# Performance work log

Hardware: AMD Instinct MI355X
Metric: run time of the kernel (lower is better)

## Reference

```python
import jax, jax.numpy as jnp
import numpy as np


def conv2d_nchw(x, w, b, padding):
    # x: [B,Cin,H,W], w: [Cout,Cin,kh,kw]
    y = jax.lax.conv_general_dilated(
        x, w, window_strides=(1, 1), padding=padding,
        dimension_numbers=("NCHW", "OIHW", "NCHW"))
    return y + b[None, :, None, None]


def setup_inputs() -> dict:
    key = jax.random.key(0)
    ks = jax.random.split(key, 8)
    B, C, H, W = 8, 512, 50, 76
    A = 9  # 3 scales x 3 ratios
    base_feat = jax.random.normal(ks[0], (B, C, H, W), dtype=jnp.float32)
    im_info = jnp.tile(jnp.array([800.0, 1216.0, 1.0], jnp.float32), (B, 1))
    gt_boxes = jax.random.uniform(ks[1], (B, 20, 5), dtype=jnp.float32) * 100.0
    num_boxes = jax.random.randint(ks[2], (B,), 1, 20, dtype=jnp.int32)
    # learned parameters (Kaiming-ish small init)
    conv_w = jax.random.normal(ks[3], (512, C, 3, 3), dtype=jnp.float32) * 0.01
    conv_b = jnp.zeros((512,), jnp.float32)
    cls_w = jax.random.normal(ks[4], (2 * A, 512, 1, 1), dtype=jnp.float32) * 0.01
    cls_b = jnp.zeros((2 * A,), jnp.float32)
    bbox_w = jax.random.normal(ks[5], (4 * A, 512, 1, 1), dtype=jnp.float32) * 0.01
    bbox_b = jnp.zeros((4 * A,), jnp.float32)
    return dict(base_feat=base_feat, im_info=im_info, gt_boxes=gt_boxes,
                num_boxes=num_boxes, conv_w=conv_w, conv_b=conv_b,
                cls_w=cls_w, cls_b=cls_b, bbox_w=bbox_w, bbox_b=bbox_b)


def reference(base_feat, im_info, gt_boxes, num_boxes,
              conv_w, conv_b, cls_w, cls_b, bbox_w, bbox_b):
    # RPN_Conv 3x3 + ReLU
    rpn_conv = jax.nn.relu(conv2d_nchw(base_feat, conv_w, conv_b, "SAME"))
    # 1x1 cls head -> [B, 2A, H, W]
    rpn_cls_score = conv2d_nchw(rpn_conv, cls_w, cls_b, "VALID")
    B, C2, H, W = rpn_cls_score.shape
    # _RPN.reshape(x, 2): view as [B, 2, A*H, W], softmax over the 2-way dim
    score_rs = rpn_cls_score.reshape(B, 2, (C2 // 2) * H, W)
    prob_rs = jax.nn.softmax(score_rs, axis=1)
    rpn_cls_prob = prob_rs.reshape(B, C2, H, W)
    # 1x1 bbox head -> [B, 4A, H, W]
    rpn_bbox_pred = conv2d_nchw(rpn_conv, bbox_w, bbox_b, "VALID")
    return rpn_cls_prob, rpn_bbox_pred
```

## Files before the change

kernel.cpp:

```cpp
#include <hip/hip_runtime.h>
#include <hip/hip_bf16.h>


typedef __bf16 bf16_t;
typedef __attribute__((ext_vector_type(8))) __bf16 bf16x8;
typedef __attribute__((ext_vector_type(4))) __bf16 bf16x4;
typedef __attribute__((ext_vector_type(4))) float f32x4;

#define HW 3800
#define XP_IMG (52 * 78 * 512)

__device__ __forceinline__ void gload_lds16(const bf16_t* g, char* l) {
  __builtin_amdgcn_global_load_lds(
      (const __attribute__((address_space(1))) unsigned int*)g,
      (__attribute__((address_space(3))) unsigned int*)l, 16, 0, 0);
}

__global__ __launch_bounds__(256) void prep_all(const float* __restrict__ x,
                                                const float* __restrict__ cw,
                                                const float* __restrict__ clsw,
                                                const float* __restrict__ boxw,
                                                bf16_t* __restrict__ Xp,
                                                bf16_t* __restrict__ Wt,
                                                bf16_t* __restrict__ WhbF) {
  __shared__ __align__(16) bf16_t tile[76][136];
  __shared__ bf16_t lw[4608];
  const int t = threadIdx.x;
  const int blk = blockIdx.x;
  if (blk < 1600) {
    const int cb = blk & 3;
    int r = blk >> 2;
    const int h = r % 50, b = r / 50;
#pragma unroll
    for (int it = 0; it < 10; ++it) {
      int idx = it * 256 + t;
      if (idx < 2432) {
        int c = idx / 19, w4 = idx - c * 19;
        const float4 v = *(const float4*)(x +
            (((size_t)(b * 512 + cb * 128 + c)) * 50 + h) * 76 + w4 * 4);
        tile[w4 * 4 + 0][c] = (bf16_t)v.x;
        tile[w4 * 4 + 1][c] = (bf16_t)v.y;
        tile[w4 * 4 + 2][c] = (bf16_t)v.z;
        tile[w4 * 4 + 3][c] = (bf16_t)v.w;
      }
    }
    __syncthreads();
#pragma unroll
    for (int it = 0; it < 5; ++it) {
      int idx = it * 256 + t;
      if (idx < 1216) {
        int w = idx >> 4, c8 = idx & 15;
        bf16x8 v = *(const bf16x8*)&tile[w][c8 * 8];
        *(bf16x8*)(Xp + ((size_t)(b * 52 + h + 1) * 78 + (w + 1)) * 512 +
                   cb * 128 + c8 * 8) = v;
      }
    }
  } else if (blk < 1616) {
    const int blk2 = blk - 1600;
    const int b = blk2 >> 1, half = blk2 & 1;
    bf16x8 z;
#pragma unroll
    for (int j = 0; j < 8; ++j) z[j] = (bf16_t)0.f;
#pragma unroll
    for (int it = 0; it < 32; ++it) {
      int idx = it * 256 + t;
      int q = half * 128 + (idx >> 6);
      int c8 = idx & 63;
      int h, w;
      if (q < 78)       { h = 0;           w = q; }
      else if (q < 156) { h = 51;          w = q - 78; }
      else if (q < 206) { h = q - 156 + 1; w = 0; }
      else              { h = q - 206 + 1; w = 77; }
      *(bf16x8*)(Xp + ((size_t)(b * 52 + h) * 78 + w) * 512 + c8 * 8) = z;
    }
  } else if (blk < 2128) {
    const int co = blk - 1616;
    const float* src = cw + (size_t)co * 4608;
#pragma unroll
    for (int it = 0; it < 18; ++it) {
      int idx = it * 256 + t;
      lw[idx] = (bf16_t)src[idx];
    }
    __syncthreads();
#pragma unroll
    for (int s = 0; s < 9; ++s) {
      int ci = t * 2;
      bf16_t v0 = lw[ci * 9 + s], v1 = lw[(ci + 1) * 9 + s];
      bf16_t* dst = Wt + ((size_t)s * 512 + co) * 512 + ci;
      dst[0] = v0; dst[1] = v1;
    }
  } else {
    int idx = (blk - 2128) * 256 + t;
    int lane = idx & 63, kt = (idx >> 6) & 15, mf = idx >> 10;
    int row = mf * 16 + (lane & 15);
    int ci0 = kt * 32 + (lane >> 4) * 8;
    bf16x8 v;
#pragma unroll
    for (int j = 0; j < 8; ++j) {
      float val = 0.f;
      if (row < 18) {
        int a = row >> 1, logit = row & 1;
        val = clsw[(logit * 9 + a) * 512 + ci0 + j];
      } else if (row < 54) {
        val = boxw[(row - 18) * 512 + ci0 + j];
      }
      v[j] = (bf16_t)val;
    }
    *(bf16x8*)(WhbF + (size_t)idx * 8) = v;
  }
}

__global__ __launch_bounds__(512) void conv_fused(const bf16_t* __restrict__ Xp,
                                                  const bf16_t* __restrict__ Wt,
                                                  const float* __restrict__ convb,
                                                  const bf16_t* __restrict__ WhbF,
                                                  const float* __restrict__ clsb,
                                                  const float* __restrict__ boxb,
                                                  float* __restrict__ out) {
  __shared__ __align__(16) char smem[131072];
  const int tid = threadIdx.x;
  const int lane = tid & 63;
  const int wv = tid >> 6;
  const int wm = wv >> 1;
  const int wn = wv & 1;
  const int lm = lane & 15, lg = lane >> 4;

  const int raw = blockIdx.x;
  const int wg = (raw & 7) * 30 + (raw >> 3);
  const int b = wg / 30;
  const int pos_base = (wg - b * 30) * 128;
  const bf16_t* XpB = Xp + (size_t)b * XP_IMG;

  int aSrc[4], aDst[4];
#pragma unroll
  for (int i = 0; i < 4; ++i) {
    int d = i * 512 + tid;
    int r = d >> 2, p = d & 3, c = p ^ ((r >> 1) & 3);
    aSrc[i] = r * 512 + c * 8;
    aDst[i] = r * 64 + p * 16;
  }
  int bSpa, bCc, bDst;
  {
    int r = tid >> 2, p = tid & 3, c = p ^ ((r >> 1) & 3);
    int m = pos_base + r; if (m > HW - 1) m = HW - 1;
    bSpa = (m / 76) * 78 + (m - (m / 76) * 76);
    bCc = c * 8;
    bDst = 32768 + r * 64 + p * 16;
  }

  const int koff = (lg ^ ((lm >> 1) & 3)) << 4;
  int aOff[8], bOff[4];
#pragma unroll
  for (int m = 0; m < 8; ++m) aOff[m] = (wm * 128 + m * 16 + lm) * 64 + koff;
#pragma unroll
  for (int n = 0; n < 4; ++n) bOff[n] = 32768 + (wn * 64 + n * 16 + lm) * 64 + koff;

  f32x4 acc[8][4];
#pragma unroll
  for (int i = 0; i < 8; ++i)
#pragma unroll
    for (int j = 0; j < 4; ++j) acc[i][j] = (f32x4){0.f, 0.f, 0.f, 0.f};

#define STAGE_A(KT, BUF) {                                                      \
    const int s_ = (KT) >> 4, cb_ = (KT) & 15;                                  \
    const bf16_t* p_ = Wt + (size_t)s_ * 262144 + cb_ * 32;                     \
    _Pragma("unroll")                                                           \
    for (int i_ = 0; i_ < 4; ++i_)                                              \
      gload_lds16(p_ + aSrc[i_], (BUF) + aDst[i_]);                             \
  }
#define STAGE_B(KT, BUF) {                                                      \
    const int s_ = (KT) >> 4, cb_ = (KT) & 15;                                  \
    const int sp_ = (s_ / 3) * 78 + (s_ - (s_ / 3) * 3);                        \
    gload_lds16(XpB + (size_t)(bSpa + sp_) * 512 + bCc + cb_ * 32,              \
                (BUF) + bDst);                                                  \
  }

  STAGE_A(0, smem)
  STAGE_B(0, smem)
  asm volatile("s_waitcnt vmcnt(0)" ::: "memory");
  __builtin_amdgcn_s_barrier();
  __builtin_amdgcn_sched_barrier(0);

  for (int kt = 0; kt < 144; ++kt) {
    const char* Ab = smem + (kt & 1) * 40960;
    char* Anxt = smem + ((kt + 1) & 1) * 40960;
    const int tn = kt + 1;
    bf16x8 pa[4], pb[4];

    if (tn < 144) STAGE_A(tn, Anxt)
#pragma unroll
    for (int n = 0; n < 4; ++n) pb[n] = *(const bf16x8*)(Ab + bOff[n]);
#pragma unroll
    for (int f = 0; f < 4; ++f) pa[f] = *(const bf16x8*)(Ab + aOff[f]);
    __builtin_amdgcn_s_setprio(1);
#pragma unroll
    for (int f = 0; f < 4; ++f)
#pragma unroll
      for (int n = 0; n < 4; ++n)
        acc[f][n] = __builtin_amdgcn_mfma_f32_16x16x32_bf16(pa[f], pb[n], acc[f][n], 0, 0, 0);
    __builtin_amdgcn_s_setprio(0);
    __builtin_amdgcn_s_barrier();

    if (tn < 144) STAGE_B(tn, Anxt)
#pragma unroll
    for (int f = 0; f < 4; ++f) pa[f] = *(const bf16x8*)(Ab + aOff[4 + f]);
    __builtin_amdgcn_s_setprio(1);
#pragma unroll
    for (int f = 0; f < 4; ++f)
#pragma unroll
      for (int n = 0; n < 4; ++n)
        acc[4 + f][n] = __builtin_amdgcn_mfma_f32_16x16x32_bf16(pa[f], pb[n], acc[4 + f][n], 0, 0, 0);
    __builtin_amdgcn_s_setprio(0);

    asm volatile("s_waitcnt vmcnt(0)" ::: "memory");
    __builtin_amdgcn_s_barrier();
    __builtin_amdgcn_sched_barrier(0);
  }
#undef STAGE_A
#undef STAGE_B

#pragma unroll
  for (int m = 0; m < 8; ++m) {
    const int co = wm * 128 + m * 16 + lg * 4;
    const float4 bias = *(const float4*)(convb + co);
    const int cb2 = co * 2;
#pragma unroll
    for (int n = 0; n < 4; ++n) {
      const int pl = wn * 64 + n * 16 + lm;
      bf16x4 v;
      float z0 = acc[m][n][0] + bias.x; v[0] = (bf16_t)(z0 > 0.f ? z0 : 0.f);
      float z1 = acc[m][n][1] + bias.y; v[1] = (bf16_t)(z1 > 0.f ? z1 : 0.f);
      float z2 = acc[m][n][2] + bias.z; v[2] = (bf16_t)(z2 > 0.f ? z2 : 0.f);
      float z3 = acc[m][n][3] + bias.w; v[3] = (bf16_t)(z3 > 0.f ? z3 : 0.f);
      *(bf16x4*)(smem + pl * 1024 + (cb2 ^ ((pl & 7) << 4))) = v;
    }
  }
  __syncthreads();

  {
    const int ps = wv * 16;
    const int prow = ps + lm;
    const int rsw = (lm & 7) << 4;
    f32x4 acc2[4];
#pragma unroll
    for (int i = 0; i < 4; ++i) acc2[i] = (f32x4){0.f, 0.f, 0.f, 0.f};
#pragma unroll
    for (int kt = 0; kt < 16; ++kt) {
      const bf16x8 bfr = *(const bf16x8*)(smem + prow * 1024 +
                                          ((kt * 64 + lg * 16) ^ rsw));
#pragma unroll
      for (int mf = 0; mf < 4; ++mf) {
        const bf16x8 af = *(const bf16x8*)(WhbF +
            ((size_t)(mf * 16 + kt) * 64 + lane) * 8);
        acc2[mf] = __builtin_amdgcn_mfma_f32_16x16x32_bf16(af, bfr, acc2[mf], 0, 0, 0);
      }
    }
    const int pos = pos_base + ps + lm;
    if (pos < HW) {
      float* boxOut = out + (size_t)8 * 18 * HW;
#pragma unroll
      for (int mf = 0; mf < 4; ++mf) {
#pragma unroll
        for (int pr = 0; pr < 2; ++pr) {
          const int row0 = mf * 16 + lg * 4 + pr * 2;
          const float v0 = acc2[mf][pr * 2];
          const float v1 = acc2[mf][pr * 2 + 1];
          if (row0 < 18) {
            const int a = row0 >> 1;
            const float s0 = v0 + clsb[a];
            const float s1 = v1 + clsb[9 + a];
            const float mx = fmaxf(s0, s1);
            const float e0 = expf(s0 - mx), e1 = expf(s1 - mx);
            const float inv = 1.0f / (e0 + e1);
            out[((size_t)(b * 18 + a)) * HW + pos] = e0 * inv;
            out[((size_t)(b * 18 + 9 + a)) * HW + pos] = e1 * inv;
          } else if (row0 < 54) {
            const int c0 = row0 - 18;
            boxOut[((size_t)(b * 36 + c0)) * HW + pos] = v0 + boxb[c0];
            boxOut[((size_t)(b * 36 + c0 + 1)) * HW + pos] = v1 + boxb[c0 + 1];
          }
        }
      }
    }
  }
}

extern "C" void kernel_launch(void* const* d_in, const int* in_sizes, int n_in,
                              void* d_out, int out_size, void* d_ws, size_t ws_size,
                              hipStream_t stream) {
  (void)in_sizes; (void)n_in; (void)out_size; (void)ws_size;
  const float* base_feat = (const float*)d_in[0];
  const float* conv_w = (const float*)d_in[4];
  const float* conv_b = (const float*)d_in[5];
  const float* cls_w  = (const float*)d_in[6];
  const float* cls_b  = (const float*)d_in[7];
  const float* bbox_w = (const float*)d_in[8];
  const float* bbox_b = (const float*)d_in[9];

  char* ws = (char*)d_ws;
  bf16_t* Xp   = (bf16_t*)(ws);
  bf16_t* Wt   = (bf16_t*)(ws + 33226752);
  bf16_t* WhbF = (bf16_t*)(ws + 37945344);

  hipLaunchKernelGGL(prep_all,   dim3(2144), dim3(256), 0, stream,
                     base_feat, conv_w, cls_w, bbox_w, Xp, Wt, WhbF);
  hipLaunchKernelGGL(conv_fused, dim3(240),  dim3(512), 0, stream,
                     Xp, Wt, conv_b, WhbF, cls_b, bbox_b, (float*)d_out);
}
```

Baseline: 163.4 us.

## Double K-tile depth to 64 with 8-way swizzle and halve loop iterations

The K step per pipeline stage grows from 32 to 64 channels. LDS buffers double to 80KB each (160KB total), the XOR swizzle widens to 8 chunks per 128-byte row, and the main loop drops from 144 to 72 iterations. Each iteration now runs four MFMA phases and splits the A staging across two of them. The aim is to amortise barriers, waitcnt stalls and loop overhead over more MFMA work per sync. The cost is a larger LDS footprint that must fit within the 160KB per-CU limit.

```diff
diff --git a/kernel.cpp b/kernel.cpp
--- a/kernel.cpp
+++ b/kernel.cpp
@@ -117,7 +117,7 @@
                                                   const float* __restrict__ clsb,
                                                   const float* __restrict__ boxb,
                                                   float* __restrict__ out) {
-  __shared__ __align__(16) char smem[131072];
+  __shared__ __align__(16) char smem[163840];
   const int tid = threadIdx.x;
   const int lane = tid & 63;
   const int wv = tid >> 6;
@@ -131,29 +131,32 @@
   const int pos_base = (wg - b * 30) * 128;
   const bf16_t* XpB = Xp + (size_t)b * XP_IMG;
 
-  int aSrc[4], aDst[4];
-#pragma unroll
-  for (int i = 0; i < 4; ++i) {
+  int aSrc[8], aDst[8];
+#pragma unroll
+  for (int i = 0; i < 8; ++i) {
     int d = i * 512 + tid;
-    int r = d >> 2, p = d & 3, c = p ^ ((r >> 1) & 3);
+    int r = d >> 3, p = d & 7, c = p ^ (r & 7);
     aSrc[i] = r * 512 + c * 8;
-    aDst[i] = r * 64 + p * 16;
-  }
-  int bSpa, bCc, bDst;
-  {
-    int r = tid >> 2, p = tid & 3, c = p ^ ((r >> 1) & 3);
+    aDst[i] = r * 128 + p * 16;
+  }
+  int bSpa[2], bCc[2], bDst[2];
+#pragma unroll
+  for (int i = 0; i < 2; ++i) {
+    int d = i * 512 + tid;
+    int r = d >> 3, p = d & 7, c = p ^ (r & 7);
     int m = pos_base + r; if (m > HW - 1) m = HW - 1;
-    bSpa = (m / 76) * 78 + (m - (m / 76) * 76);
-    bCc = c * 8;
-    bDst = 32768 + r * 64 + p * 16;
-  }
-
-  const int koff = (lg ^ ((lm >> 1) & 3)) << 4;
-  int aOff[8], bOff[4];
-#pragma unroll
-  for (int m = 0; m < 8; ++m) aOff[m] = (wm * 128 + m * 16 + lm) * 64 + koff;
-#pragma unroll
-  for (int n = 0; n < 4; ++n) bOff[n] = 32768 + (wn * 64 + n * 16 + lm) * 64 + koff;
+    bSpa[i] = (m / 76) * 78 + (m - (m / 76) * 76);
+    bCc[i] = c * 8;
+    bDst[i] = 65536 + r * 128 + p * 16;
+  }
+
+  int aOff[8], bOff[4], koffs[2];
+#pragma unroll
+  for (int m = 0; m < 8; ++m) aOff[m] = (wm * 128 + m * 16 + lm) * 128;
+#pragma unroll
+  for (int n = 0; n < 4; ++n) bOff[n] = 65536 + (wn * 64 + n * 16 + lm) * 128;
+#pragma unroll
+  for (int ks = 0; ks < 2; ++ks) koffs[ks] = ((ks * 4 + lg) ^ (lm & 7)) << 4;
 
   f32x4 acc[8][4];
 #pragma unroll
@@ -161,37 +164,40 @@
 #pragma unroll
     for (int j = 0; j < 4; ++j) acc[i][j] = (f32x4){0.f, 0.f, 0.f, 0.f};
 
-#define STAGE_A(KT, BUF) {                                                      \
-    const int s_ = (KT) >> 4, cb_ = (KT) & 15;                                  \
-    const bf16_t* p_ = Wt + (size_t)s_ * 262144 + cb_ * 32;                     \
+#define STAGE_A(KT, BUF, I0, I1) {                                              \
+    const int s_ = (KT) >> 3, cb_ = (KT) & 7;                                   \
+    const bf16_t* p_ = Wt + (size_t)s_ * 262144 + cb_ * 64;                     \
     _Pragma("unroll")                                                           \
-    for (int i_ = 0; i_ < 4; ++i_)                                              \
+    for (int i_ = (I0); i_ < (I1); ++i_)                                        \
       gload_lds16(p_ + aSrc[i_], (BUF) + aDst[i_]);                             \
   }
 #define STAGE_B(KT, BUF) {                                                      \
-    const int s_ = (KT) >> 4, cb_ = (KT) & 15;                                  \
+    const int s_ = (KT) >> 3, cb_ = (KT) & 7;                                   \
     const int sp_ = (s_ / 3) * 78 + (s_ - (s_ / 3) * 3);                        \
-    gload_lds16(XpB + (size_t)(bSpa + sp_) * 512 + bCc + cb_ * 32,              \
-                (BUF) + bDst);                                                  \
-  }
-
-  STAGE_A(0, smem)
+    _Pragma("unroll")                                                           \
+    for (int i_ = 0; i_ < 2; ++i_)                                              \
+      gload_lds16(XpB + (size_t)(bSpa[i_] + sp_) * 512 + bCc[i_] + cb_ * 64,    \
+                  (BUF) + bDst[i_]);                                            \
+  }
+
+  STAGE_A(0, smem, 0, 8)
   STAGE_B(0, smem)
   asm volatile("s_waitcnt vmcnt(0)" ::: "memory");
   __builtin_amdgcn_s_barrier();
   __builtin_amdgcn_sched_barrier(0);
 
-  for (int kt = 0; kt < 144; ++kt) {
-    const char* Ab = smem + (kt & 1) * 40960;
-    char* Anxt = smem + ((kt + 1) & 1) * 40960;
+  for (int kt = 0; kt < 72; ++kt) {
+    const char* Ab = smem + (kt & 1) * 81920;
+    char* Anxt = smem + ((kt + 1) & 1) * 81920;
     const int tn = kt + 1;
+    const bool more = (tn < 72);
     bf16x8 pa[4], pb[4];
 
-    if (tn < 144) STAGE_A(tn, Anxt)
-#pragma unroll
-    for (int n = 0; n < 4; ++n) pb[n] = *(const bf16x8*)(Ab + bOff[n]);
-#pragma unroll
-    for (int f = 0; f < 4; ++f) pa[f] = *(const bf16x8*)(Ab + aOff[f]);
+    if (more) STAGE_A(tn, Anxt, 0, 4)
+#pragma unroll
+    for (int n = 0; n < 4; ++n) pb[n] = *(const bf16x8*)(Ab + bOff[n] + koffs[0]);
+#pragma unroll
+    for (int f = 0; f < 4; ++f) pa[f] = *(const bf16x8*)(Ab + aOff[f] + koffs[0]);
     __builtin_amdgcn_s_setprio(1);
 #pragma unroll
     for (int f = 0; f < 4; ++f)
@@ -201,9 +207,34 @@
     __builtin_amdgcn_s_setprio(0);
     __builtin_amdgcn_s_barrier();
 
-    if (tn < 144) STAGE_B(tn, Anxt)
-#pragma unroll
-    for (int f = 0; f < 4; ++f) pa[f] = *(const bf16x8*)(Ab + aOff[4 + f]);
+    if (more) STAGE_A(tn, Anxt, 4, 8)
+#pragma unroll
+    for (int f = 0; f < 4; ++f) pa[f] = *(const bf16x8*)(Ab + aOff[4 + f] + koffs[0]);
+    __builtin_amdgcn_s_setprio(1);
+#pragma unroll
+    for (int f = 0; f < 4; ++f)
+#pragma unroll
+      for (int n = 0; n < 4; ++n)
+        acc[4 + f][n] = __builtin_amdgcn_mfma_f32_16x16x32_bf16(pa[f], pb[n], acc[4 + f][n], 0, 0, 0);
+    __builtin_amdgcn_s_setprio(0);
+    __builtin_amdgcn_s_barrier();
+
+    if (more) STAGE_B(tn, Anxt)
+#pragma unroll
+    for (int n = 0; n < 4; ++n) pb[n] = *(const bf16x8*)(Ab + bOff[n] + koffs[1]);
+#pragma unroll
+    for (int f = 0; f < 4; ++f) pa[f] = *(const bf16x8*)(Ab + aOff[f] + koffs[1]);
+    __builtin_amdgcn_s_setprio(1);
+#pragma unroll
+    for (int f = 0; f < 4; ++f)
+#pragma unroll
+      for (int n = 0; n < 4; ++n)
+        acc[f][n] = __builtin_amdgcn_mfma_f32_16x16x32_bf16(pa[f], pb[n], acc[f][n], 0, 0, 0);
+    __builtin_amdgcn_s_setprio(0);
+    __builtin_amdgcn_s_barrier();
+
+#pragma unroll
+    for (int f = 0; f < 4; ++f) pa[f] = *(const bf16x8*)(Ab + aOff[4 + f] + koffs[1]);
     __builtin_amdgcn_s_setprio(1);
 #pragma unroll
     for (int f = 0; f < 4; ++f)
```

Measured after the change: 150.5 us, median of 2. 1.09x faster.
